# Kernel optimization log

Measured on AMD Instinct MI355X. Metric: run time of the kernel, lower is better.

## Reference

```python
import jax, jax.numpy as jnp
import numpy as np

N_NODES = 200000
N_EVENTS = 200000
MEM_DIM = 128
MSG_DIM = 128
TIME_DIM = 16
MSG_IN = 2 * MEM_DIM + MSG_DIM + TIME_DIM  # 400


def setup_inputs() -> dict:
    key = jax.random.key(0)
    ks = jax.random.split(key, 12)
    return {
        "src_ids": jax.random.randint(ks[0], (N_EVENTS,), 0, N_NODES, dtype=jnp.int32),
        "dst_ids": jax.random.randint(ks[1], (N_EVENTS,), 0, N_NODES, dtype=jnp.int32),
        "edge_feat": jax.random.normal(ks[2], (N_EVENTS, MSG_DIM), dtype=jnp.float32),
        "timestamps": jax.random.uniform(ks[3], (N_EVENTS,), dtype=jnp.float32),
        "memory": jax.random.normal(ks[4], (N_NODES, MEM_DIM), dtype=jnp.float32) * 0.1,
        "last_update_time": jnp.zeros((N_NODES,), dtype=jnp.float32),
        "time_w": jax.random.normal(ks[5], (TIME_DIM,), dtype=jnp.float32),
        "time_phi": jnp.zeros((TIME_DIM,), dtype=jnp.float32),
        "W1": jax.random.normal(ks[6], (MSG_IN, MSG_DIM), dtype=jnp.float32) / np.sqrt(MSG_IN),
        "b1": jnp.zeros((MSG_DIM,), dtype=jnp.float32),
        "W2": jax.random.normal(ks[7], (MSG_DIM, MSG_DIM), dtype=jnp.float32) / np.sqrt(MSG_DIM),
        "b2": jnp.zeros((MSG_DIM,), dtype=jnp.float32),
        "W_ih": jax.random.normal(ks[8], (3 * MEM_DIM, MSG_DIM), dtype=jnp.float32) / np.sqrt(MSG_DIM),
        "W_hh": jax.random.normal(ks[9], (3 * MEM_DIM, MEM_DIM), dtype=jnp.float32) / np.sqrt(MEM_DIM),
        "b_ih": jnp.zeros((3 * MEM_DIM,), dtype=jnp.float32),
        "b_hh": jnp.zeros((3 * MEM_DIM,), dtype=jnp.float32),
    }


def _time_encode(dt, w, phi):
    # Time2Vec: linear first channel, sin on the rest
    wt = dt[:, None] * w[None, :] + phi[None, :]  # [E, TIME_DIM]
    return jnp.concatenate([wt[:, :1], jnp.sin(wt[:, 1:])], axis=-1)


def _message_mlp(x, W1, b1, W2, b2):
    h = jax.nn.relu(x @ W1 + b1)
    return h @ W2 + b2


def _gru_cell(x, h, W_ih, W_hh, b_ih, b_hh):
    gi = x @ W_ih.T + b_ih  # [U, 3H]
    gh = h @ W_hh.T + b_hh
    i_r, i_z, i_n = jnp.split(gi, 3, axis=-1)
    h_r, h_z, h_n = jnp.split(gh, 3, axis=-1)
    r = jax.nn.sigmoid(i_r + h_r)
    z = jax.nn.sigmoid(i_z + h_z)
    n = jnp.tanh(i_n + r * h_n)
    return (1.0 - z) * n + z * h


def reference(src_ids, dst_ids, edge_feat, timestamps, memory, last_update_time,
              time_w, time_phi, W1, b1, W2, b2, W_ih, W_hh, b_ih, b_hh):
    # 1) gather + time encode
    dt_src = timestamps - last_update_time[src_ids]
    dt_dst = timestamps - last_update_time[dst_ids]
    te_src = _time_encode(dt_src, time_w, time_phi)
    te_dst = _time_encode(dt_dst, time_w, time_phi)
    src_mem = memory[src_ids]
    dst_mem = memory[dst_ids]

    # 2) messages
    msg_src = _message_mlp(jnp.concatenate([src_mem, dst_mem, edge_feat, te_src], -1), W1, b1, W2, b2)
    msg_dst = _message_mlp(jnp.concatenate([dst_mem, src_mem, edge_feat, te_dst], -1), W1, b1, W2, b2)

    all_nodes = jnp.concatenate([src_ids, dst_ids])  # [2E]
    all_msgs = jnp.concatenate([msg_src, msg_dst], axis=0)  # [2E, MSG_DIM]

    # 3) 'last' aggregation: segment-max of positions, then gather
    pos = jnp.arange(all_nodes.shape[0], dtype=jnp.int32)
    last_pos = jax.ops.segment_max(pos, all_nodes, num_segments=N_NODES)  # int32 min where absent
    present = last_pos >= 0  # [N]
    agg = all_msgs[jnp.clip(last_pos, 0, None)]  # [N, MSG_DIM]
    agg = jnp.where(present[:, None], agg, 0.0)

    # 4) GRU memory update on involved nodes only
    new_mem = _gru_cell(agg, memory, W_ih, W_hh, b_ih, b_hh)
    memory_out = jnp.where(present[:, None], new_mem, memory)
    return memory_out
```

## Files before the change

### kernel.cpp

```cpp
#include <hip/hip_runtime.h>
#include <hip/hip_bf16.h>
#include <math.h>

#define NN 200000
#define NE 200000

typedef __attribute__((ext_vector_type(8))) short bf16x8;
typedef __attribute__((ext_vector_type(4))) float f32x4;

#define XASTR 136
#define XBSTR 296
#define OSTR  132
#define NT    (NN / 32)
#define PBT   (32 * XBSTR)

__device__ __forceinline__ float sigm(float x) { return 1.0f / (1.0f + __expf(-x)); }
__device__ __forceinline__ float tanh_f(float x) {
    float e = __expf(2.0f * x);
    return 1.0f - 2.0f / (e + 1.0f);
}
__device__ __forceinline__ ushort f2b(float x) {
    union { __hip_bfloat16 b; ushort u; } v;
    v.b = __float2bfloat16(x);
    return v.u;
}
__device__ __forceinline__ float b2f(ushort u) {
    return __uint_as_float(((unsigned)u) << 16);
}
__device__ __forceinline__ ushort4 cvt4(float4 v) {
    ushort4 u; u.x = f2b(v.x); u.y = f2b(v.y); u.z = f2b(v.z); u.w = f2b(v.w);
    return u;
}
__device__ __forceinline__ void gload_lds16(const ushort* g, ushort* l) {
    __builtin_amdgcn_global_load_lds(
        (const __attribute__((address_space(1))) unsigned int*)g,
        (__attribute__((address_space(3))) unsigned int*)l, 16, 0, 0);
}

#define MFMA16(a, b, c) __builtin_amdgcn_mfma_f32_16x16x32_bf16((a), (b), (c), 0, 0, 0)

__global__ void k_scatter(const int* __restrict__ src, const int* __restrict__ dst,
                          int* __restrict__ last_pos) {
    int i = blockIdx.x * blockDim.x + threadIdx.x;
    if (i < NE) {
        atomicMax(&last_pos[src[i]], i);
    } else if (i < 2 * NE) {
        atomicMax(&last_pos[dst[i - NE]], i);
    }
}

#define NB_PREP 594
#define NB_GATH (NN / 16)
__global__ __launch_bounds__(256)
void k_pg(const float* __restrict__ W1, const float* __restrict__ W2,
          const float* __restrict__ Wih, const float* __restrict__ Whh,
          const float* __restrict__ b2, const float* __restrict__ bih,
          ushort* __restrict__ W1F, ushort* __restrict__ W2IF,
          ushort* __restrict__ WHF, float* __restrict__ cb,
          const int* __restrict__ last_pos,
          const int* __restrict__ src, const int* __restrict__ dst,
          const float* __restrict__ ts, const float* __restrict__ lut,
          const float* __restrict__ mem, const float* __restrict__ ef,
          const float* __restrict__ tw, const float* __restrict__ tphi,
          ushort* __restrict__ PB, float* __restrict__ out)
{
    int b = blockIdx.x;
    if (b < NB_PREP) {
        int t = b * 256 + threadIdx.x;
        if (t < 104 * 512) {
            int f = t >> 9, idx = t & 511;
            int lane = idx >> 3, j = idx & 7, c16 = lane & 15, k8 = lane >> 4;
            int wvv = f / 26, r = f % 26, kt = r >> 1, ns = r & 1;
            int col = wvv * 32 + ns * 16 + c16;
            int kk = kt * 32 + k8 * 8 + j;
            W1F[t] = (kk < 400) ? f2b(W1[kk * 128 + col]) : (ushort)0;
            return;
        }
        t -= 104 * 512;
        if (t < 96 * 512) {
            int f = t >> 9, idx = t & 511;
            int lane = idx >> 3, j = idx & 7, c16 = lane & 15, k8 = lane >> 4;
            int wvv = f / 24, r = f % 24, kt = r / 6, rem = r % 6, g = rem >> 1, ns = rem & 1;
            int col = g * 128 + wvv * 32 + ns * 16 + c16;
            int kk = kt * 32 + k8 * 8 + j;
            float s = 0.0f;
            for (int c = 0; c < 128; ++c) s = fmaf(W2[kk * 128 + c], Wih[col * 128 + c], s);
            W2IF[f * 512 + idx] = f2b(s);
            return;
        }
        t -= 96 * 512;
        if (t < 96 * 512) {
            int f = t >> 9, idx = t & 511;
            int lane = idx >> 3, j = idx & 7, c16 = lane & 15, k8 = lane >> 4;
            int wvv = f / 24, r = f % 24, kt = r / 6, rem = r % 6, g = rem >> 1, ns = rem & 1;
            int col = g * 128 + wvv * 32 + ns * 16 + c16;
            int kk = kt * 32 + k8 * 8 + j;
            WHF[f * 512 + idx] = f2b(Whh[col * 128 + kk]);
            return;
        }
        t -= 96 * 512;
        if (t < 384) {
            float s = bih[t];
            for (int k = 0; k < 128; ++k) s = fmaf(b2[k], Wih[t * 128 + k], s);
            cb[t] = s;
        }
        return;
    }

    const int wv = threadIdx.x >> 6, lane = threadIdx.x & 63;
    const int n0 = (((b - NB_PREP) * 4) + wv) * 4;
    const int l = lane & 31;
    const bool lo = lane < 32;

    int p[4];
    #pragma unroll
    for (int s = 0; s < 4; ++s) p[s] = last_pos[n0 + s];

    float4 mv[4], fv[4];
    float te[4];
    #pragma unroll
    for (int s = 0; s < 4; ++s) {
        te[s] = 0.0f;
        if (p[s] >= 0) {
            int e = (p[s] < NE) ? p[s] : p[s] - NE;
            int o = (p[s] < NE) ? dst[e] : src[e];
            if (lo) {
                mv[s] = *(const float4*)&mem[(size_t)o * 128 + l * 4];
                if (l < 16) {
                    float dt = ts[e] - lut[n0 + s];
                    float w = fmaf(dt, tw[l], tphi[l]);
                    te[s] = (l == 0) ? w : __sinf(w);
                }
            } else {
                fv[s] = *(const float4*)&ef[(size_t)e * 128 + l * 4];
            }
        }
    }
    #pragma unroll
    for (int s = 0; s < 4; ++s) {
        if (p[s] >= 0) {
            ushort* xb = PB + (size_t)(n0 + s) * XBSTR;
            if (lo) {
                *(ushort4*)&xb[l * 4] = cvt4(mv[s]);
                xb[256 + l] = (l < 16) ? f2b(te[s]) : (ushort)0;
            } else {
                *(ushort4*)&xb[128 + l * 4] = cvt4(fv[s]);
            }
        } else {
            float2 v = *(const float2*)&mem[(size_t)(n0 + s) * 128 + lane * 2];
            *(float2*)&out[(size_t)(n0 + s) * 128 + lane * 2] = v;
        }
    }
}

__global__ __launch_bounds__(256, 4)
void k_main10(const ushort* __restrict__ PB, const int* __restrict__ last_pos,
              const float* __restrict__ mem,
              const ushort* __restrict__ W1F, const float* __restrict__ b1,
              const ushort* __restrict__ W2IF, const ushort* __restrict__ WHF,
              const float* __restrict__ cb, const float* __restrict__ bhh,
              float* __restrict__ out)
{
    __shared__ __align__(16) ushort XA[32 * XASTR];
    __shared__ __align__(16) ushort HB[32 * XASTR];
    __shared__ __align__(16) ushort XB[32 * XBSTR];
    __shared__ unsigned char pres[32];

    const int tile = (NT - 1) - blockIdx.x;
    const int base = tile * 32;
    const int tid  = threadIdx.x;
    const int lane = tid & 63;
    const int wv   = tid >> 6;
    const int r16  = lane & 15;
    const int kb   = lane >> 4;

    {
        const ushort* srcPB = PB + (size_t)tile * PBT;
        #pragma unroll
        for (int j = 0; j < 5; ++j) {
            int cc = wv + j * 4;
            if (cc < 18) gload_lds16(srcPB + cc * 512 + lane * 8, XB + cc * 512);
            else if (cc == 18 && lane < 32) gload_lds16(srcPB + cc * 512 + lane * 8, XB + cc * 512);
        }
    }
    {
        const float* msrc = mem + (size_t)base * 128;
        #pragma unroll
        for (int k = 0; k < 4; ++k) {
            int i0 = k * 1024 + tid * 4;
            float4 v = *(const float4*)&msrc[i0];
            *(ushort4*)&XA[(i0 >> 7) * XASTR + (i0 & 127)] = cvt4(v);
        }
        if (tid < 32) pres[tid] = (unsigned char)(last_pos[base + tid] >= 0);
    }
    const ushort* w1 = W1F  + wv * (26 * 512) + lane * 8;
    const ushort* wI = W2IF + wv * (24 * 512) + lane * 8;
    const ushort* wH = WHF  + wv * (24 * 512) + lane * 8;
    __syncthreads();

    f32x4 c1[2][2] = {};
    {
        const ushort* aA = &XA[r16 * XASTR + kb * 8];
        const ushort* aB = &XB[r16 * XBSTR + kb * 8];
        bf16x8 p0[4], p1[4];
        #pragma unroll
        for (int q = 0; q < 4; ++q) {
            p0[q] = *(const bf16x8*)(w1 + (q * 2 + 0) * 512);
            p1[q] = *(const bf16x8*)(w1 + (q * 2 + 1) * 512);
        }
        #pragma unroll
        for (int kt = 0; kt < 13; ++kt) {
            const ushort* ap  = (kt < 4) ? (aA + kt * 32) : (aB + (kt - 4) * 32);
            const int     ast = (kt < 4) ? XASTR : XBSTR;
            bf16x8 A0 = *(const bf16x8*)ap;
            bf16x8 A1 = *(const bf16x8*)(ap + 16 * ast);
            bf16x8 B0 = p0[kt & 3];
            bf16x8 B1 = p1[kt & 3];
            c1[0][0] = MFMA16(A0, B0, c1[0][0]);
            c1[0][1] = MFMA16(A0, B1, c1[0][1]);
            c1[1][0] = MFMA16(A1, B0, c1[1][0]);
            c1[1][1] = MFMA16(A1, B1, c1[1][1]);
            if (kt + 4 < 13) {
                p0[kt & 3] = *(const bf16x8*)(w1 + ((kt + 4) * 2 + 0) * 512);
                p1[kt & 3] = *(const bf16x8*)(w1 + ((kt + 4) * 2 + 1) * 512);
            }
        }
    }
    #pragma unroll
    for (int ns = 0; ns < 2; ++ns) {
        int col = wv * 32 + ns * 16 + r16;
        float bb = b1[col];
        #pragma unroll
        for (int m = 0; m < 2; ++m)
            #pragma unroll
            for (int r = 0; r < 4; ++r)
                HB[(m * 16 + kb * 4 + r) * XASTR + col] =
                    f2b(fmaxf(c1[m][ns][r] + bb, 0.0f));
    }
    __syncthreads();

    float* XBf = (float*)XB;
    #pragma unroll
    for (int ns = 0; ns < 2; ++ns) {
        f32x4 arz[2][2] = {};
        f32x4 an_i[2] = {};
        f32x4 an_h[2] = {};
        const ushort* am = &HB[r16 * XASTR + kb * 8];
        const ushort* ah = &XA[r16 * XASTR + kb * 8];
        bf16x8 pi[4], ph[4];
        #pragma unroll
        for (int q = 0; q < 4; ++q) {
            int kt = q / 3, s = q % 3;
            int fo = (kt * 6 + s * 2 + ns) * 512;
            pi[q] = *(const bf16x8*)(wI + fo);
            ph[q] = *(const bf16x8*)(wH + fo);
        }
        #pragma unroll
        for (int q = 0; q < 12; ++q) {
            int kt = q / 3, s = q % 3;
            bf16x8 M0 = *(const bf16x8*)(am + kt * 32);
            bf16x8 M1 = *(const bf16x8*)(am + 16 * XASTR + kt * 32);
            bf16x8 H0 = *(const bf16x8*)(ah + kt * 32);
            bf16x8 H1 = *(const bf16x8*)(ah + 16 * XASTR + kt * 32);
            bf16x8 Bi = pi[q & 3];
            bf16x8 Bh = ph[q & 3];
            if (s < 2) {
                arz[0][s] = MFMA16(M0, Bi, arz[0][s]);
                arz[0][s] = MFMA16(H0, Bh, arz[0][s]);
                arz[1][s] = MFMA16(M1, Bi, arz[1][s]);
                arz[1][s] = MFMA16(H1, Bh, arz[1][s]);
            } else {
                an_i[0] = MFMA16(M0, Bi, an_i[0]);
                an_i[1] = MFMA16(M1, Bi, an_i[1]);
                an_h[0] = MFMA16(H0, Bh, an_h[0]);
                an_h[1] = MFMA16(H1, Bh, an_h[1]);
            }
            if (q + 4 < 12) {
                int kq = (q + 4) / 3, sq = (q + 4) % 3;
                int fo = (kq * 6 + sq * 2 + ns) * 512;
                pi[q & 3] = *(const bf16x8*)(wI + fo);
                ph[q & 3] = *(const bf16x8*)(wH + fo);
            }
        }
        {
            int col = wv * 32 + ns * 16 + r16;
            float brz0 = cb[col] + bhh[col];
            float brz1 = cb[128 + col] + bhh[128 + col];
            float bin  = cb[256 + col];
            float bhn  = bhh[256 + col];
            #pragma unroll
            for (int m = 0; m < 2; ++m) {
                #pragma unroll
                for (int r = 0; r < 4; ++r) {
                    int row = m * 16 + kb * 4 + r;
                    float rr = sigm(arz[m][0][r] + brz0);
                    float zz = sigm(arz[m][1][r] + brz1);
                    float nn = tanh_f(an_i[m][r] + bin + rr * (an_h[m][r] + bhn));
                    float hh = b2f(XA[row * XASTR + col]);
                    XBf[row * OSTR + col] = fmaf(zz, hh - nn, nn);
                }
            }
        }
    }
    __syncthreads();

    for (int j = wv; j < 32; j += 4) {
        if (pres[j]) {
            float2 v = *(const float2*)&XBf[j * OSTR + lane * 2];
            *(float2*)&out[(size_t)(base + j) * 128 + lane * 2] = v;
        }
    }
}

extern "C" void kernel_launch(void* const* d_in, const int* in_sizes, int n_in,
                              void* d_out, int out_size, void* d_ws, size_t ws_size,
                              hipStream_t stream) {
    const int*   src  = (const int*)d_in[0];
    const int*   dst  = (const int*)d_in[1];
    const float* ef   = (const float*)d_in[2];
    const float* ts   = (const float*)d_in[3];
    const float* mem  = (const float*)d_in[4];
    const float* lut  = (const float*)d_in[5];
    const float* tw   = (const float*)d_in[6];
    const float* tphi = (const float*)d_in[7];
    const float* W1   = (const float*)d_in[8];
    const float* b1   = (const float*)d_in[9];
    const float* W2   = (const float*)d_in[10];
    const float* b2   = (const float*)d_in[11];
    const float* Wih  = (const float*)d_in[12];
    const float* Whh  = (const float*)d_in[13];
    const float* bih  = (const float*)d_in[14];
    const float* bhh  = (const float*)d_in[15];
    float* out = (float*)d_out;

    char* ws = (char*)d_ws;
    size_t off = 0;
    int*    last_pos = (int*)(ws + off);    off += (size_t)NN * 4;
    ushort* W1F      = (ushort*)(ws + off); off += (size_t)104 * 512 * 2;
    ushort* W2IF     = (ushort*)(ws + off); off += (size_t)96 * 512 * 2;
    ushort* WHF      = (ushort*)(ws + off); off += (size_t)96 * 512 * 2;
    float*  cb       = (float*)(ws + off);  off += (size_t)384 * 4 + 64;
    ushort* PB       = (ushort*)(ws + off);

    hipMemsetAsync(last_pos, 0xFF, (size_t)NN * sizeof(int), stream);

    k_scatter<<<(2 * NE + 255) / 256, 256, 0, stream>>>(src, dst, last_pos);
    k_pg<<<NB_PREP + NB_GATH, 256, 0, stream>>>(
        W1, W2, Wih, Whh, b2, bih, W1F, W2IF, WHF, cb,
        last_pos, src, dst, ts, lut, mem, ef, tw, tphi, PB, out);
    k_main10<<<NT, 256, 0, stream>>>(PB, last_pos, mem, W1F, b1, W2IF, WHF, cb, bhh, out);
}
```

Before: 229.2 us.

## Make main kernel persistent with register-resident weights and double-buffered tile prefetch

The main MLP+GRU kernel becomes persistent: a fixed grid of 256 blocks each loops over many 32-node tiles. All fragments of W1, W_ih and W_hh are loaded once into registers per wave instead of being streamed from global memory for every tile. The next tile's packed inputs and memory rows are prefetched into a second LDS buffer while the current tile computes. This removes repeated weight loads and per-block launch and prologue cost, but it needs very many registers (74 bf16x8 vectors, so occupancy is limited to one block per CU) and leaves less latency hiding between waves.

```diff
diff --git a/kernel.cpp b/kernel.cpp
--- a/kernel.cpp
+++ b/kernel.cpp
@@ -13,6 +13,7 @@
 #define OSTR  132
 #define NT    (NN / 32)
 #define PBT   (32 * XBSTR)
+#define GRID_MAIN 256
 
 __device__ __forceinline__ float sigm(float x) { return 1.0f / (1.0f + __expf(-x)); }
 __device__ __forceinline__ float tanh_f(float x) {
@@ -153,162 +154,193 @@
     }
 }
 
-__global__ __launch_bounds__(256, 4)
-void k_main10(const ushort* __restrict__ PB, const int* __restrict__ last_pos,
+__global__ __launch_bounds__(256, 1)
+void k_main12(const ushort* __restrict__ PB, const int* __restrict__ last_pos,
               const float* __restrict__ mem,
               const ushort* __restrict__ W1F, const float* __restrict__ b1,
               const ushort* __restrict__ W2IF, const ushort* __restrict__ WHF,
               const float* __restrict__ cb, const float* __restrict__ bhh,
               float* __restrict__ out)
 {
-    __shared__ __align__(16) ushort XA[32 * XASTR];
+    __shared__ __align__(16) ushort XAd[2][32 * XASTR];
+    __shared__ __align__(16) ushort XBd[2][32 * XBSTR];
     __shared__ __align__(16) ushort HB[32 * XASTR];
-    __shared__ __align__(16) ushort XB[32 * XBSTR];
-    __shared__ unsigned char pres[32];
-
-    const int tile = (NT - 1) - blockIdx.x;
-    const int base = tile * 32;
+    __shared__ unsigned char presd[2][32];
+
     const int tid  = threadIdx.x;
     const int lane = tid & 63;
     const int wv   = tid >> 6;
     const int r16  = lane & 15;
     const int kb   = lane >> 4;
 
+    bf16x8 W1r[26], WIr[24], WHr[24];
     {
-        const ushort* srcPB = PB + (size_t)tile * PBT;
-        #pragma unroll
-        for (int j = 0; j < 5; ++j) {
-            int cc = wv + j * 4;
-            if (cc < 18) gload_lds16(srcPB + cc * 512 + lane * 8, XB + cc * 512);
-            else if (cc == 18 && lane < 32) gload_lds16(srcPB + cc * 512 + lane * 8, XB + cc * 512);
-        }
-    }
-    {
-        const float* msrc = mem + (size_t)base * 128;
-        #pragma unroll
-        for (int k = 0; k < 4; ++k) {
-            int i0 = k * 1024 + tid * 4;
-            float4 v = *(const float4*)&msrc[i0];
-            *(ushort4*)&XA[(i0 >> 7) * XASTR + (i0 & 127)] = cvt4(v);
-        }
-        if (tid < 32) pres[tid] = (unsigned char)(last_pos[base + tid] >= 0);
-    }
-    const ushort* w1 = W1F  + wv * (26 * 512) + lane * 8;
-    const ushort* wI = W2IF + wv * (24 * 512) + lane * 8;
-    const ushort* wH = WHF  + wv * (24 * 512) + lane * 8;
-    __syncthreads();
-
-    f32x4 c1[2][2] = {};
-    {
-        const ushort* aA = &XA[r16 * XASTR + kb * 8];
-        const ushort* aB = &XB[r16 * XBSTR + kb * 8];
-        bf16x8 p0[4], p1[4];
-        #pragma unroll
-        for (int q = 0; q < 4; ++q) {
-            p0[q] = *(const bf16x8*)(w1 + (q * 2 + 0) * 512);
-            p1[q] = *(const bf16x8*)(w1 + (q * 2 + 1) * 512);
-        }
-        #pragma unroll
-        for (int kt = 0; kt < 13; ++kt) {
-            const ushort* ap  = (kt < 4) ? (aA + kt * 32) : (aB + (kt - 4) * 32);
-            const int     ast = (kt < 4) ? XASTR : XBSTR;
-            bf16x8 A0 = *(const bf16x8*)ap;
-            bf16x8 A1 = *(const bf16x8*)(ap + 16 * ast);
-            bf16x8 B0 = p0[kt & 3];
-            bf16x8 B1 = p1[kt & 3];
-            c1[0][0] = MFMA16(A0, B0, c1[0][0]);
-            c1[0][1] = MFMA16(A0, B1, c1[0][1]);
-            c1[1][0] = MFMA16(A1, B0, c1[1][0]);
-            c1[1][1] = MFMA16(A1, B1, c1[1][1]);
-            if (kt + 4 < 13) {
-                p0[kt & 3] = *(const bf16x8*)(w1 + ((kt + 4) * 2 + 0) * 512);
-                p1[kt & 3] = *(const bf16x8*)(w1 + ((kt + 4) * 2 + 1) * 512);
-            }
-        }
-    }
+        const ushort* w1 = W1F  + wv * (26 * 512) + lane * 8;
+        #pragma unroll
+        for (int i = 0; i < 26; ++i) W1r[i] = *(const bf16x8*)(w1 + i * 512);
+        const ushort* wI = W2IF + wv * (24 * 512) + lane * 8;
+        const ushort* wH = WHF  + wv * (24 * 512) + lane * 8;
+        #pragma unroll
+        for (int i = 0; i < 24; ++i) {
+            WIr[i] = *(const bf16x8*)(wI + i * 512);
+            WHr[i] = *(const bf16x8*)(wH + i * 512);
+        }
+    }
+    float b1v[2], brz0[2], brz1[2], binv[2], bhnv[2];
     #pragma unroll
     for (int ns = 0; ns < 2; ++ns) {
         int col = wv * 32 + ns * 16 + r16;
-        float bb = b1[col];
-        #pragma unroll
-        for (int m = 0; m < 2; ++m)
-            #pragma unroll
-            for (int r = 0; r < 4; ++r)
-                HB[(m * 16 + kb * 4 + r) * XASTR + col] =
-                    f2b(fmaxf(c1[m][ns][r] + bb, 0.0f));
-    }
-    __syncthreads();
-
-    float* XBf = (float*)XB;
-    #pragma unroll
-    for (int ns = 0; ns < 2; ++ns) {
-        f32x4 arz[2][2] = {};
-        f32x4 an_i[2] = {};
-        f32x4 an_h[2] = {};
-        const ushort* am = &HB[r16 * XASTR + kb * 8];
-        const ushort* ah = &XA[r16 * XASTR + kb * 8];
-        bf16x8 pi[4], ph[4];
-        #pragma unroll
-        for (int q = 0; q < 4; ++q) {
-            int kt = q / 3, s = q % 3;
-            int fo = (kt * 6 + s * 2 + ns) * 512;
-            pi[q] = *(const bf16x8*)(wI + fo);
-            ph[q] = *(const bf16x8*)(wH + fo);
-        }
-        #pragma unroll
-        for (int q = 0; q < 12; ++q) {
-            int kt = q / 3, s = q % 3;
-            bf16x8 M0 = *(const bf16x8*)(am + kt * 32);
-            bf16x8 M1 = *(const bf16x8*)(am + 16 * XASTR + kt * 32);
-            bf16x8 H0 = *(const bf16x8*)(ah + kt * 32);
-            bf16x8 H1 = *(const bf16x8*)(ah + 16 * XASTR + kt * 32);
-            bf16x8 Bi = pi[q & 3];
-            bf16x8 Bh = ph[q & 3];
-            if (s < 2) {
-                arz[0][s] = MFMA16(M0, Bi, arz[0][s]);
-                arz[0][s] = MFMA16(H0, Bh, arz[0][s]);
-                arz[1][s] = MFMA16(M1, Bi, arz[1][s]);
-                arz[1][s] = MFMA16(H1, Bh, arz[1][s]);
-            } else {
-                an_i[0] = MFMA16(M0, Bi, an_i[0]);
-                an_i[1] = MFMA16(M1, Bi, an_i[1]);
-                an_h[0] = MFMA16(H0, Bh, an_h[0]);
-                an_h[1] = MFMA16(H1, Bh, an_h[1]);
-            }
-            if (q + 4 < 12) {
-                int kq = (q + 4) / 3, sq = (q + 4) % 3;
-                int fo = (kq * 6 + sq * 2 + ns) * 512;
-                pi[q & 3] = *(const bf16x8*)(wI + fo);
-                ph[q & 3] = *(const bf16x8*)(wH + fo);
-            }
-        }
+        b1v[ns]  = b1[col];
+        brz0[ns] = cb[col] + bhh[col];
+        brz1[ns] = cb[128 + col] + bhh[128 + col];
+        binv[ns] = cb[256 + col];
+        bhnv[ns] = bhh[256 + col];
+    }
+
+    const int t0 = blockIdx.x;
+    {
+        const int tile = (NT - 1) - t0;
+        const int base = tile * 32;
+        const float* msrc = mem + (size_t)base * 128;
+        float4 xa[4];
+        #pragma unroll
+        for (int k = 0; k < 4; ++k) xa[k] = *(const float4*)&msrc[k * 1024 + tid * 4];
+        int pr = (tid < 32) ? last_pos[base + tid] : -1;
+        const ushort* srcPB = PB + (size_t)tile * PBT;
+        #pragma unroll
+        for (int j = 0; j < 5; ++j) {
+            int cc = wv + j * 4;
+            if (cc < 18) gload_lds16(srcPB + cc * 512 + lane * 8, &XBd[0][cc * 512]);
+            else if (cc == 18 && lane < 32) gload_lds16(srcPB + cc * 512 + lane * 8, &XBd[0][cc * 512]);
+        }
+        #pragma unroll
+        for (int k = 0; k < 4; ++k) {
+            int i0 = k * 1024 + tid * 4;
+            *(ushort4*)&XAd[0][(i0 >> 7) * XASTR + (i0 & 127)] = cvt4(xa[k]);
+        }
+        if (tid < 32) presd[0][tid] = (unsigned char)(pr >= 0);
+        asm volatile("s_waitcnt vmcnt(0)" ::: "memory");
+        __syncthreads();
+    }
+
+    int c = 0;
+    for (int t = t0; t < NT; t += GRID_MAIN) {
+        const int tile = (NT - 1) - t;
+        const int base = tile * 32;
+        const int tn = t + GRID_MAIN;
+        const ushort* XA = XAd[c];
+        const ushort* XB = XBd[c];
+
+        f32x4 c1[2][2] = {};
         {
+            const ushort* aA = &XA[r16 * XASTR + kb * 8];
+            const ushort* aB = &XB[r16 * XBSTR + kb * 8];
+            #pragma unroll
+            for (int kt = 0; kt < 13; ++kt) {
+                const ushort* ap  = (kt < 4) ? (aA + kt * 32) : (aB + (kt - 4) * 32);
+                const int     ast = (kt < 4) ? XASTR : XBSTR;
+                bf16x8 A0 = *(const bf16x8*)ap;
+                bf16x8 A1 = *(const bf16x8*)(ap + 16 * ast);
+                c1[0][0] = MFMA16(A0, W1r[kt * 2 + 0], c1[0][0]);
+                c1[0][1] = MFMA16(A0, W1r[kt * 2 + 1], c1[0][1]);
+                c1[1][0] = MFMA16(A1, W1r[kt * 2 + 0], c1[1][0]);
+                c1[1][1] = MFMA16(A1, W1r[kt * 2 + 1], c1[1][1]);
+            }
+        }
+        #pragma unroll
+        for (int ns = 0; ns < 2; ++ns) {
             int col = wv * 32 + ns * 16 + r16;
-            float brz0 = cb[col] + bhh[col];
-            float brz1 = cb[128 + col] + bhh[128 + col];
-            float bin  = cb[256 + col];
-            float bhn  = bhh[256 + col];
+            #pragma unroll
+            for (int m = 0; m < 2; ++m)
+                #pragma unroll
+                for (int r = 0; r < 4; ++r)
+                    HB[(m * 16 + kb * 4 + r) * XASTR + col] =
+                        f2b(fmaxf(c1[m][ns][r] + b1v[ns], 0.0f));
+        }
+        __syncthreads();
+
+        float4 xan[4];
+        int prn = -1;
+        if (tn < NT) {
+            const int nbase = ((NT - 1) - tn) * 32;
+            const float* msrc = mem + (size_t)nbase * 128;
+            #pragma unroll
+            for (int k = 0; k < 4; ++k) xan[k] = *(const float4*)&msrc[k * 1024 + tid * 4];
+            if (tid < 32) prn = last_pos[nbase + tid];
+            const ushort* srcPB = PB + (size_t)((NT - 1) - tn) * PBT;
+            #pragma unroll
+            for (int j = 0; j < 5; ++j) {
+                int cc = wv + j * 4;
+                if (cc < 18) gload_lds16(srcPB + cc * 512 + lane * 8, &XBd[c ^ 1][cc * 512]);
+                else if (cc == 18 && lane < 32) gload_lds16(srcPB + cc * 512 + lane * 8, &XBd[c ^ 1][cc * 512]);
+            }
+        }
+
+        float* XBf = (float*)XBd[c];
+        #pragma unroll
+        for (int ns = 0; ns < 2; ++ns) {
+            f32x4 arz[2][2] = {};
+            f32x4 an_i[2] = {};
+            f32x4 an_h[2] = {};
+            const ushort* am = &HB[r16 * XASTR + kb * 8];
+            const ushort* ah = &XA[r16 * XASTR + kb * 8];
+            #pragma unroll
+            for (int kt = 0; kt < 4; ++kt) {
+                bf16x8 M0 = *(const bf16x8*)(am + kt * 32);
+                bf16x8 M1 = *(const bf16x8*)(am + 16 * XASTR + kt * 32);
+                bf16x8 H0 = *(const bf16x8*)(ah + kt * 32);
+                bf16x8 H1 = *(const bf16x8*)(ah + 16 * XASTR + kt * 32);
+                #pragma unroll
+                for (int s = 0; s < 3; ++s) {
+                    bf16x8 Bi = WIr[kt * 6 + s * 2 + ns];
+                    bf16x8 Bh = WHr[kt * 6 + s * 2 + ns];
+                    if (s < 2) {
+                        arz[0][s] = MFMA16(M0, Bi, arz[0][s]);
+                        arz[0][s] = MFMA16(H0, Bh, arz[0][s]);
+                        arz[1][s] = MFMA16(M1, Bi, arz[1][s]);
+                        arz[1][s] = MFMA16(H1, Bh, arz[1][s]);
+                    } else {
+                        an_i[0] = MFMA16(M0, Bi, an_i[0]);
+                        an_i[1] = MFMA16(M1, Bi, an_i[1]);
+                        an_h[0] = MFMA16(H0, Bh, an_h[0]);
+                        an_h[1] = MFMA16(H1, Bh, an_h[1]);
+                    }
+                }
+            }
             #pragma unroll
             for (int m = 0; m < 2; ++m) {
                 #pragma unroll
                 for (int r = 0; r < 4; ++r) {
                     int row = m * 16 + kb * 4 + r;
-                    float rr = sigm(arz[m][0][r] + brz0);
-                    float zz = sigm(arz[m][1][r] + brz1);
-                    float nn = tanh_f(an_i[m][r] + bin + rr * (an_h[m][r] + bhn));
+                    int col = wv * 32 + ns * 16 + r16;
+                    float rr = sigm(arz[m][0][r] + brz0[ns]);
+                    float zz = sigm(arz[m][1][r] + brz1[ns]);
+                    float nn = tanh_f(an_i[m][r] + binv[ns] + rr * (an_h[m][r] + bhnv[ns]));
                     float hh = b2f(XA[row * XASTR + col]);
                     XBf[row * OSTR + col] = fmaf(zz, hh - nn, nn);
                 }
             }
         }
-    }
-    __syncthreads();
-
-    for (int j = wv; j < 32; j += 4) {
-        if (pres[j]) {
-            float2 v = *(const float2*)&XBf[j * OSTR + lane * 2];
-            *(float2*)&out[(size_t)(base + j) * 128 + lane * 2] = v;
-        }
+        __syncthreads();
+
+        for (int j = wv; j < 32; j += 4) {
+            if (presd[c][j]) {
+                float2 v = *(const float2*)&XBf[j * OSTR + lane * 2];
+                *(float2*)&out[(size_t)(base + j) * 128 + lane * 2] = v;
+            }
+        }
+
+        if (tn < NT) {
+            #pragma unroll
+            for (int k = 0; k < 4; ++k) {
+                int i0 = k * 1024 + tid * 4;
+                *(ushort4*)&XAd[c ^ 1][(i0 >> 7) * XASTR + (i0 & 127)] = cvt4(xan[k]);
+            }
+            if (tid < 32) presd[c ^ 1][tid] = (unsigned char)(prn >= 0);
+        }
+        asm volatile("s_waitcnt vmcnt(0)" ::: "memory");
+        __syncthreads();
+        c ^= 1;
     }
 }
 
@@ -348,5 +380,6 @@
     k_pg<<<NB_PREP + NB_GATH, 256, 0, stream>>>(
         W1, W2, Wih, Whh, b2, bih, W1F, W2IF, WHF, cb,
         last_pos, src, dst, ts, lut, mem, ef, tw, tphi, PB, out);
-    k_main10<<<NT, 256, 0, stream>>>(PB, last_pos, mem, W1F, b1, W2IF, WHF, cb, bhh, out);
-}
+    k_main12<<<GRID_MAIN, 256, 0, stream>>>(PB, last_pos, mem, W1F, b1, W2IF, WHF,
+                                            cb, bhh, out);
+}
```

Result: slower. 264.0 us (+15.2%).

## Double main-kernel row tile and feed memory fragments directly from global

Applied to the files above, without the earlier changes.

The fused MLP+GRU kernel now processes 64 nodes per block instead of 32, so each weight fragment loaded from global feeds four MFMA row groups instead of two. The memory rows are no longer staged into LDS; A fragments are loaded from global and converted to bf16 in registers, both for the first layer and for the hidden-state GEMM. The hidden activations reuse the staging buffer. Output is written straight from registers for present rows, which drops the final LDS round-trip and barrier. In exchange, the memory tile is read from global twice plus once more for the fp32 blend. The weight prefetch ring is gone and register pressure rises under the 4-block launch bound, which could cause spills.

```diff
diff --git a/kernel.cpp b/kernel.cpp
--- a/kernel.cpp
+++ b/kernel.cpp
@@ -8,11 +8,10 @@
 typedef __attribute__((ext_vector_type(8))) short bf16x8;
 typedef __attribute__((ext_vector_type(4))) float f32x4;
 
-#define XASTR 136
 #define XBSTR 296
-#define OSTR  132
-#define NT    (NN / 32)
-#define PBT   (32 * XBSTR)
+#define MR    64
+#define NT64  (NN / MR)
+#define PBT64 (MR * XBSTR)
 
 __device__ __forceinline__ float sigm(float x) { return 1.0f / (1.0f + __expf(-x)); }
 __device__ __forceinline__ float tanh_f(float x) {
@@ -24,12 +23,17 @@
     v.b = __float2bfloat16(x);
     return v.u;
 }
-__device__ __forceinline__ float b2f(ushort u) {
-    return __uint_as_float(((unsigned)u) << 16);
-}
 __device__ __forceinline__ ushort4 cvt4(float4 v) {
     ushort4 u; u.x = f2b(v.x); u.y = f2b(v.y); u.z = f2b(v.z); u.w = f2b(v.w);
     return u;
+}
+__device__ __forceinline__ bf16x8 ldAfrag(const float* p) {
+    float4 a = *(const float4*)p;
+    float4 b = *(const float4*)(p + 4);
+    union { ushort4 u4[2]; bf16x8 v; } r;
+    r.u4[0] = cvt4(a);
+    r.u4[1] = cvt4(b);
+    return r.v;
 }
 __device__ __forceinline__ void gload_lds16(const ushort* g, ushort* l) {
     __builtin_amdgcn_global_load_lds(
@@ -154,20 +158,18 @@
 }
 
 __global__ __launch_bounds__(256, 4)
-void k_main10(const ushort* __restrict__ PB, const int* __restrict__ last_pos,
+void k_main13(const ushort* __restrict__ PB, const int* __restrict__ last_pos,
               const float* __restrict__ mem,
               const ushort* __restrict__ W1F, const float* __restrict__ b1,
               const ushort* __restrict__ W2IF, const ushort* __restrict__ WHF,
               const float* __restrict__ cb, const float* __restrict__ bhh,
               float* __restrict__ out)
 {
-    __shared__ __align__(16) ushort XA[32 * XASTR];
-    __shared__ __align__(16) ushort HB[32 * XASTR];
-    __shared__ __align__(16) ushort XB[32 * XBSTR];
-    __shared__ unsigned char pres[32];
-
-    const int tile = (NT - 1) - blockIdx.x;
-    const int base = tile * 32;
+    __shared__ __align__(16) ushort XB[MR * XBSTR];
+    __shared__ unsigned char pres[MR];
+
+    const int tile = (NT64 - 1) - blockIdx.x;
+    const int base = tile * MR;
     const int tid  = threadIdx.x;
     const int lane = tid & 63;
     const int wv   = tid >> 6;
@@ -175,111 +177,90 @@
     const int kb   = lane >> 4;
 
     {
-        const ushort* srcPB = PB + (size_t)tile * PBT;
+        const ushort* srcPB = PB + (size_t)tile * PBT64;
         #pragma unroll
-        for (int j = 0; j < 5; ++j) {
+        for (int j = 0; j < 10; ++j) {
             int cc = wv + j * 4;
-            if (cc < 18) gload_lds16(srcPB + cc * 512 + lane * 8, XB + cc * 512);
-            else if (cc == 18 && lane < 32) gload_lds16(srcPB + cc * 512 + lane * 8, XB + cc * 512);
-        }
-    }
-    {
-        const float* msrc = mem + (size_t)base * 128;
-        #pragma unroll
-        for (int k = 0; k < 4; ++k) {
-            int i0 = k * 1024 + tid * 4;
-            float4 v = *(const float4*)&msrc[i0];
-            *(ushort4*)&XA[(i0 >> 7) * XASTR + (i0 & 127)] = cvt4(v);
-        }
-        if (tid < 32) pres[tid] = (unsigned char)(last_pos[base + tid] >= 0);
-    }
+            if (cc < 37) gload_lds16(srcPB + cc * 512 + lane * 8, XB + cc * 512);
+        }
+    }
+    if (tid < MR) pres[tid] = (unsigned char)(last_pos[base + tid] >= 0);
+
     const ushort* w1 = W1F  + wv * (26 * 512) + lane * 8;
     const ushort* wI = W2IF + wv * (24 * 512) + lane * 8;
     const ushort* wH = WHF  + wv * (24 * 512) + lane * 8;
+    const float*  mbase = mem + (size_t)base * 128 + r16 * 128 + kb * 8;
     __syncthreads();
 
-    f32x4 c1[2][2] = {};
+    f32x4 c1[4][2] = {};
     {
-        const ushort* aA = &XA[r16 * XASTR + kb * 8];
         const ushort* aB = &XB[r16 * XBSTR + kb * 8];
-        bf16x8 p0[4], p1[4];
-        #pragma unroll
-        for (int q = 0; q < 4; ++q) {
-            p0[q] = *(const bf16x8*)(w1 + (q * 2 + 0) * 512);
-            p1[q] = *(const bf16x8*)(w1 + (q * 2 + 1) * 512);
-        }
         #pragma unroll
         for (int kt = 0; kt < 13; ++kt) {
-            const ushort* ap  = (kt < 4) ? (aA + kt * 32) : (aB + (kt - 4) * 32);
-            const int     ast = (kt < 4) ? XASTR : XBSTR;
-            bf16x8 A0 = *(const bf16x8*)ap;
-            bf16x8 A1 = *(const bf16x8*)(ap + 16 * ast);
-            bf16x8 B0 = p0[kt & 3];
-            bf16x8 B1 = p1[kt & 3];
-            c1[0][0] = MFMA16(A0, B0, c1[0][0]);
-            c1[0][1] = MFMA16(A0, B1, c1[0][1]);
-            c1[1][0] = MFMA16(A1, B0, c1[1][0]);
-            c1[1][1] = MFMA16(A1, B1, c1[1][1]);
-            if (kt + 4 < 13) {
-                p0[kt & 3] = *(const bf16x8*)(w1 + ((kt + 4) * 2 + 0) * 512);
-                p1[kt & 3] = *(const bf16x8*)(w1 + ((kt + 4) * 2 + 1) * 512);
-            }
-        }
-    }
+            bf16x8 A[4];
+            if (kt < 4) {
+                #pragma unroll
+                for (int rg = 0; rg < 4; ++rg) A[rg] = ldAfrag(mbase + rg * 2048 + kt * 32);
+            } else {
+                #pragma unroll
+                for (int rg = 0; rg < 4; ++rg)
+                    A[rg] = *(const bf16x8*)(aB + rg * 16 * XBSTR + (kt - 4) * 32);
+            }
+            bf16x8 B0 = *(const bf16x8*)(w1 + (kt * 2 + 0) * 512);
+            bf16x8 B1 = *(const bf16x8*)(w1 + (kt * 2 + 1) * 512);
+            #pragma unroll
+            for (int rg = 0; rg < 4; ++rg) {
+                c1[rg][0] = MFMA16(A[rg], B0, c1[rg][0]);
+                c1[rg][1] = MFMA16(A[rg], B1, c1[rg][1]);
+            }
+        }
+    }
+    __syncthreads();
+
     #pragma unroll
     for (int ns = 0; ns < 2; ++ns) {
         int col = wv * 32 + ns * 16 + r16;
         float bb = b1[col];
         #pragma unroll
-        for (int m = 0; m < 2; ++m)
+        for (int m = 0; m < 4; ++m)
             #pragma unroll
             for (int r = 0; r < 4; ++r)
-                HB[(m * 16 + kb * 4 + r) * XASTR + col] =
+                XB[(m * 16 + kb * 4 + r) * XBSTR + 128 + col] =
                     f2b(fmaxf(c1[m][ns][r] + bb, 0.0f));
     }
     __syncthreads();
 
-    float* XBf = (float*)XB;
     #pragma unroll
     for (int ns = 0; ns < 2; ++ns) {
-        f32x4 arz[2][2] = {};
-        f32x4 an_i[2] = {};
-        f32x4 an_h[2] = {};
-        const ushort* am = &HB[r16 * XASTR + kb * 8];
-        const ushort* ah = &XA[r16 * XASTR + kb * 8];
-        bf16x8 pi[4], ph[4];
+        f32x4 arz[4][2] = {};
+        f32x4 an_i[4] = {};
+        f32x4 an_h[4] = {};
+        const ushort* am = &XB[r16 * XBSTR + 128 + kb * 8];
         #pragma unroll
-        for (int q = 0; q < 4; ++q) {
-            int kt = q / 3, s = q % 3;
-            int fo = (kt * 6 + s * 2 + ns) * 512;
-            pi[q] = *(const bf16x8*)(wI + fo);
-            ph[q] = *(const bf16x8*)(wH + fo);
-        }
-        #pragma unroll
-        for (int q = 0; q < 12; ++q) {
-            int kt = q / 3, s = q % 3;
-            bf16x8 M0 = *(const bf16x8*)(am + kt * 32);
-            bf16x8 M1 = *(const bf16x8*)(am + 16 * XASTR + kt * 32);
-            bf16x8 H0 = *(const bf16x8*)(ah + kt * 32);
-            bf16x8 H1 = *(const bf16x8*)(ah + 16 * XASTR + kt * 32);
-            bf16x8 Bi = pi[q & 3];
-            bf16x8 Bh = ph[q & 3];
-            if (s < 2) {
-                arz[0][s] = MFMA16(M0, Bi, arz[0][s]);
-                arz[0][s] = MFMA16(H0, Bh, arz[0][s]);
-                arz[1][s] = MFMA16(M1, Bi, arz[1][s]);
-                arz[1][s] = MFMA16(H1, Bh, arz[1][s]);
-            } else {
-                an_i[0] = MFMA16(M0, Bi, an_i[0]);
-                an_i[1] = MFMA16(M1, Bi, an_i[1]);
-                an_h[0] = MFMA16(H0, Bh, an_h[0]);
-                an_h[1] = MFMA16(H1, Bh, an_h[1]);
-            }
-            if (q + 4 < 12) {
-                int kq = (q + 4) / 3, sq = (q + 4) % 3;
-                int fo = (kq * 6 + sq * 2 + ns) * 512;
-                pi[q & 3] = *(const bf16x8*)(wI + fo);
-                ph[q & 3] = *(const bf16x8*)(wH + fo);
+        for (int kt = 0; kt < 4; ++kt) {
+            bf16x8 Hf[4], Gf[4];
+            #pragma unroll
+            for (int rg = 0; rg < 4; ++rg) {
+                Hf[rg] = *(const bf16x8*)(am + rg * 16 * XBSTR + kt * 32);
+                Gf[rg] = ldAfrag(mbase + rg * 2048 + kt * 32);
+            }
+            #pragma unroll
+            for (int s = 0; s < 3; ++s) {
+                bf16x8 Bi = *(const bf16x8*)(wI + (kt * 6 + s * 2 + ns) * 512);
+                bf16x8 Bh = *(const bf16x8*)(wH + (kt * 6 + s * 2 + ns) * 512);
+                if (s < 2) {
+                    #pragma unroll
+                    for (int rg = 0; rg < 4; ++rg) {
+                        arz[rg][s] = MFMA16(Hf[rg], Bi, arz[rg][s]);
+                        arz[rg][s] = MFMA16(Gf[rg], Bh, arz[rg][s]);
+                    }
+                } else {
+                    #pragma unroll
+                    for (int rg = 0; rg < 4; ++rg) {
+                        an_i[rg] = MFMA16(Hf[rg], Bi, an_i[rg]);
+                        an_h[rg] = MFMA16(Gf[rg], Bh, an_h[rg]);
+                    }
+                }
             }
         }
         {
@@ -289,25 +270,19 @@
             float bin  = cb[256 + col];
             float bhn  = bhh[256 + col];
             #pragma unroll
-            for (int m = 0; m < 2; ++m) {
+            for (int m = 0; m < 4; ++m) {
                 #pragma unroll
                 for (int r = 0; r < 4; ++r) {
                     int row = m * 16 + kb * 4 + r;
-                    float rr = sigm(arz[m][0][r] + brz0);
-                    float zz = sigm(arz[m][1][r] + brz1);
-                    float nn = tanh_f(an_i[m][r] + bin + rr * (an_h[m][r] + bhn));
-                    float hh = b2f(XA[row * XASTR + col]);
-                    XBf[row * OSTR + col] = fmaf(zz, hh - nn, nn);
+                    if (pres[row]) {
+                        float rr = sigm(arz[m][0][r] + brz0);
+                        float zz = sigm(arz[m][1][r] + brz1);
+                        float nn = tanh_f(an_i[m][r] + bin + rr * (an_h[m][r] + bhn));
+                        float hh = mem[(size_t)(base + row) * 128 + col];
+                        out[(size_t)(base + row) * 128 + col] = fmaf(zz, hh - nn, nn);
+                    }
                 }
             }
-        }
-    }
-    __syncthreads();
-
-    for (int j = wv; j < 32; j += 4) {
-        if (pres[j]) {
-            float2 v = *(const float2*)&XBf[j * OSTR + lane * 2];
-            *(float2*)&out[(size_t)(base + j) * 128 + lane * 2] = v;
         }
     }
 }
@@ -348,5 +323,6 @@
     k_pg<<<NB_PREP + NB_GATH, 256, 0, stream>>>(
         W1, W2, Wih, Whh, b2, bih, W1F, W2IF, WHF, cb,
         last_pos, src, dst, ts, lut, mem, ef, tw, tphi, PB, out);
-    k_main10<<<NT, 256, 0, stream>>>(PB, last_pos, mem, W1F, b1, W2IF, WHF, cb, bhh, out);
-}
+    k_main13<<<NT64, 256, 0, stream>>>(PB, last_pos, mem, W1F, b1, W2IF, WHF,
+                                       cb, bhh, out);
+}
```

After: 432.5 us. 1.89x slower.
